# Kernel optimization log

Hardware: AMD Instinct MI355X
Metric: run time of the kernel (lower is better)

The kernel has to match this reference:

```python
import jax, jax.numpy as jnp
import numpy as np

N, E, Z, C, B, G, T = 10000, 160000, 10, 64, 8, 16, 2
R_MAX = 5.0
AVG_NEIGH = 16.0
L_SLICES = ((0, 1), (1, 4), (4, 9))  # l=0,1,2 blocks of the 9 SH components


def sph_harm(u):
    # component-normalized real spherical harmonics up to l=2, u: [E,3] unit vectors
    x, y, z = u[:, 0], u[:, 1], u[:, 2]
    s3, s5, s15 = 3.0 ** 0.5, 5.0 ** 0.5, 15.0 ** 0.5
    return jnp.stack([
        jnp.ones_like(x),
        s3 * x, s3 * y, s3 * z,
        s15 * x * y, s15 * y * z, (s5 / 2) * (3 * z * z - 1), s15 * x * z, (s15 / 2) * (x * x - y * y),
    ], axis=1)  # [E,9]


def radial_embed(r):
    # Bessel basis * polynomial cutoff (p=5), r: [E]
    u = r / R_MAX
    n = jnp.arange(1, B + 1, dtype=jnp.float32)
    bessel = jnp.sqrt(2.0 / R_MAX) * jnp.sin(n[None, :] * jnp.pi * u[:, None]) / (r[:, None] + 1e-9)
    p = 5.0
    fc = 1 - (p + 1) * (p + 2) / 2 * u ** p + p * (p + 2) * u ** (p + 1) - p * (p + 1) / 2 * u ** (p + 2)
    fc = jnp.where(u < 1.0, fc, 0.0)
    return bessel * fc[:, None]  # [E,B]


def per_l_linear(x, W):
    # x: [n,C,9], W: [3,C,C]; independent channel mixing per l-block
    return jnp.concatenate([
        jnp.einsum('ncm,cd->ndm', x[:, :, s:e], W[l]) for l, (s, e) in enumerate(L_SLICES)
    ], axis=2)


def _forward(positions, node_attrs, charges, shifts, W_emb, atomic_energies,
             W_r1, W_r2, W_mix, W_sc, w_poly, W_prod, w_e, w_d,
             edge_index, batch, num_graphs):
    sender, receiver = edge_index[0], edge_index[1]
    # atomic reference energies
    node_e0 = node_attrs @ atomic_energies  # [N]
    e0 = jax.ops.segment_sum(node_e0, batch, num_segments=num_graphs)
    # node embedding: scalars only
    node_feats = jnp.zeros((positions.shape[0], C, 9), positions.dtype)
    node_feats = node_feats.at[:, :, 0].set(node_attrs @ W_emb)
    # edge geometry
    vec = positions[sender] - positions[receiver] + shifts  # [E,3]
    lengths = jnp.sqrt(jnp.sum(vec * vec, axis=1) + 1e-12)
    sh = sph_harm(vec / lengths[:, None])        # [E,9]
    edge_feats = radial_embed(lengths)           # [E,B]
    energies = [e0]
    dipoles = []
    for t in range(T):
        # radial MLP -> per-channel TP weights
        w = jax.nn.silu(edge_feats @ W_r1[t]) @ W_r2[t]      # [E,C]
        h_s = node_feats[sender, :, 0]                       # gather sender scalars [E,C]
        m = (w * h_s)[:, :, None] * sh[:, None, :]           # TP message [E,C,9]
        agg = jax.ops.segment_sum(m, receiver, num_segments=positions.shape[0]) / AVG_NEIGH
        msg = per_l_linear(agg, W_mix[t])
        sc = per_l_linear(node_feats, W_sc[t])               # self-connection
        # product basis (correlation 3): channel-wise scalar polynomial gate
        s0 = msg[:, :, 0]
        poly = w_poly[t, :, 0][None] + w_poly[t, :, 1][None] * s0 + w_poly[t, :, 2][None] * s0 * s0
        node_feats = per_l_linear(msg * poly[:, :, None], W_prod[t]) + sc
        # readout: 1x0e energy + 1x1o dipole
        e_n = node_feats[:, :, 0] @ w_e[t]                   # [N]
        energies.append(jax.ops.segment_sum(e_n, batch, num_segments=num_graphs))
        dipoles.append(jnp.einsum('ncm,c->nm', node_feats[:, :, 1:4], w_d[t]))  # [N,3]
    contributions = jnp.stack(energies, axis=-1)             # [G,T+1]
    total_energy = jnp.sum(contributions, axis=-1)           # [G]
    atomic_dipoles = jnp.sum(jnp.stack(dipoles, axis=-1), axis=-1)  # [N,3]
    total_dipole = jax.ops.segment_sum(atomic_dipoles, batch, num_segments=num_graphs)
    total_dipole = total_dipole + jax.ops.segment_sum(charges[:, None] * positions, batch, num_segments=num_graphs)
    return total_energy, contributions, atomic_dipoles, total_dipole


def setup_inputs():
    key = jax.random.key(0)
    ks = jax.random.split(key, 16)
    s = 0.1
    species = jax.random.randint(ks[1], (N,), 0, Z)
    return {
        'positions': jax.random.normal(ks[0], (N, 3)) * 3.0,
        'node_attrs': jax.nn.one_hot(species, Z, dtype=jnp.float32),
        'charges': jax.random.normal(ks[2], (N,)) * 0.1,
        'shifts': jnp.zeros((E, 3), jnp.float32),
        'W_emb': jax.random.normal(ks[5], (Z, C)) * s,
        'atomic_energies': jax.random.normal(ks[6], (Z,)) * s,
        'W_r1': jax.random.normal(ks[7], (T, B, 64)) * s,
        'W_r2': jax.random.normal(ks[8], (T, 64, C)) * s,
        'W_mix': jax.random.normal(ks[9], (T, 3, C, C)) * s,
        'W_sc': jax.random.normal(ks[10], (T, 3, C, C)) * s,
        'w_poly': jax.random.normal(ks[11], (T, C, 3)) * s,
        'W_prod': jax.random.normal(ks[12], (T, 3, C, C)) * s,
        'w_e': jax.random.normal(ks[13], (T, C)) * s,
        'w_d': jax.random.normal(ks[14], (T, C)) * s,
        'edge_index': jax.random.randint(ks[3], (2, E), 0, N),
        'batch': jnp.sort(jax.random.randint(ks[4], (N,), 0, G)),
        'num_graphs': G,
    }


def reference(positions, node_attrs, charges, shifts, W_emb, atomic_energies,
              W_r1, W_r2, W_mix, W_sc, w_poly, W_prod, w_e, w_d,
              edge_index, batch, num_graphs):
    args = (node_attrs, charges, shifts, W_emb, atomic_energies, W_r1, W_r2,
            W_mix, W_sc, w_poly, W_prod, w_e, w_d, edge_index, batch, num_graphs)
    total_energy, contributions, atomic_dipoles, total_dipole = _forward(positions, *args)
    forces = -jax.grad(lambda p: jnp.sum(_forward(p, *args)[0]))(positions)
    return total_energy, contributions, forces, total_dipole, atomic_dipoles
```

## Files before the change

### kernel.cpp

```cpp
#include <hip/hip_runtime.h>
#include <hip/hip_bf16.h>

#define NN 10000
#define NE 160000
#define NZ 10
#define NBES 8
#define NG 16
#define NT 2
#define NB 2048
#define NB1 2049
#define PL ((size_t)NN*64)

static constexpr float PI_F  = 3.14159265358979323846f;
static constexpr float KBES  = 0.63245553203367587f;
static constexpr float S3    = 1.73205080756887729f;

static constexpr size_t OFF_UVL  = 0;
static constexpr size_t OFF_PIN  = OFF_UVL + (size_t)NE*4;
static constexpr size_t OFF_ATT  = OFF_PIN + (size_t)NN*3;
static constexpr size_t OFF_CHG  = OFF_ATT + (size_t)NN*NZ;
static constexpr size_t OFF_SHF  = OFF_CHG + (size_t)NN;
static constexpr size_t OFF_NF0  = OFF_SHF + (size_t)NE*3;
static constexpr size_t OFF_NF1  = OFF_NF0 + PL;
static constexpr size_t OFF_MSG0 = OFF_NF1 + 4*PL;
static constexpr size_t OFF_MSG1 = OFF_MSG0 + 4*PL;
static constexpr size_t OFF_AGG  = OFF_MSG1 + 4*PL;
static constexpr size_t O_GA1    = OFF_AGG;
static constexpr size_t O_GA0    = OFF_AGG + 2*PL;
static constexpr size_t OFF_W    = OFF_AGG + 4*PL;
static constexpr size_t O_WEMB   = OFF_W;
static constexpr size_t O_AE     = O_WEMB + 640;
static constexpr size_t O_R1     = O_AE   + 16;
static constexpr size_t O_R2     = O_R1   + 1024;
static constexpr size_t O_WMIX   = O_R2   + 8192;
static constexpr size_t O_WMIXT  = O_WMIX + 24576;
static constexpr size_t O_WSC    = O_WMIXT+ 24576;
static constexpr size_t O_WSCT   = O_WSC  + 24576;
static constexpr size_t O_WPROD  = O_WSCT + 24576;
static constexpr size_t O_WPRODT = O_WPROD+ 24576;
static constexpr size_t O_WPOLY  = O_WPRODT+24576;
static constexpr size_t O_WE     = O_WPOLY+ 384;
static constexpr size_t O_WD     = O_WE   + 128;
static constexpr size_t OFF_ACC  = O_WD   + 128;
static constexpr size_t O_E0G    = OFF_ACC;
static constexpr size_t O_ETG    = O_E0G + 16;
static constexpr size_t O_TD     = O_ETG + 32;
static constexpr size_t O_ADP    = O_TD  + 48;
static constexpr size_t O_GPOS   = O_ADP + (size_t)NN*3;
static constexpr size_t ACC_FLOATS = 96 + (size_t)NN*6;
static constexpr size_t O_EN0    = O_GPOS + (size_t)NN*3;
static constexpr size_t O_EN1    = O_EN0 + NN;
static constexpr size_t O_E0N    = O_EN1 + NN;
static constexpr size_t O_FLAG   = O_E0N + NN;
static constexpr size_t O_TW     = O_FLAG + 4;
static constexpr size_t O_TQ     = O_TW + (size_t)2*NB1*64;
static constexpr size_t O_OFFR   = O_TQ + (size_t)2*NB1*64;
static constexpr size_t O_OFFS   = O_OFFR + (NN+1);
static constexpr size_t O_CURR   = O_OFFS + (NN+1);
static constexpr size_t O_CURS   = O_CURR + NN;
static constexpr size_t O_RECRAW = O_CURS + NN;
static constexpr size_t O_RECR   = (O_RECRAW + 7) & ~(size_t)7;
static constexpr size_t O_RECS   = O_RECR + (size_t)NE*8;
static constexpr size_t WS_FLOATS= O_RECS + (size_t)NE*8;

__device__ __forceinline__ float rlane(float v, int l){
  return __int_as_float(__builtin_amdgcn_readlane(__float_as_int(v), l));
}

static constexpr int LD_CNT[14] = {NN*3, NN*NZ, NN, NE*3, NZ*64, NZ, NT*NBES*64, NT*64*64,
                                   NT*3*64*64, NT*3*64*64, NT*64*3, NT*3*64*64, NT*64, NT*64};
static constexpr int LD_TOTAL = NN*3 + NN*NZ + NN + NE*3 + NZ*64 + NZ + NT*NBES*64 + NT*64*64
                              + 3*(NT*3*64*64) + NT*64*3 + 4*(NT*64) - NT*64*2;
__global__ __launch_bounds__(256) void k_load_all(
    const void* s0, const void* s1, const void* s2, const void* s3, const void* s4,
    const void* s5, const void* s6, const void* s7, const void* s8, const void* s9,
    const void* s10, const void* s11, const void* s12, const void* s13,
    float* __restrict__ ws){
  __shared__ int found;
  if (threadIdx.x == 0) found = 0;
  __syncthreads();
  const unsigned* raw = (const unsigned*)s1;
  int f = 0;
  for (int i = threadIdx.x; i < 4096; i += 256){
    unsigned w = raw[i];
    f |= (w == 0x00003F80u || w == 0x3F803F80u) ? 1 : 0;
  }
  if (f) found = 1;
  __syncthreads();
  const int isbf = found;
  if (blockIdx.x == 0 && threadIdx.x == 0) ((int*)(ws + O_FLAG))[0] = isbf;

  const void* srcs[14] = {s0,s1,s2,s3,s4,s5,s6,s7,s8,s9,s10,s11,s12,s13};
  const size_t dsts[14] = {OFF_PIN, OFF_ATT, OFF_CHG, OFF_SHF, O_WEMB, O_AE, O_R1, O_R2,
                           O_WMIX, O_WSC, O_WPOLY, O_WPROD, O_WE, O_WD};
  int i = blockIdx.x*256 + threadIdx.x;
  int seg = -1, off = i;
  #pragma unroll
  for (int j = 0; j < 14; ++j){
    if (seg < 0){
      if (off < LD_CNT[j]) seg = j;
      else off -= LD_CNT[j];
    }
  }
  if (seg < 0) return;
  float v = isbf ? __bfloat162float(((const __hip_bfloat16*)srcs[seg])[off])
                 : ((const float*)srcs[seg])[off];
  ws[dsts[seg] + off] = v;
}

__global__ void k_transpose_all(float* __restrict__ ws){
  const size_t srcs[3] = {O_WMIX, O_WSC, O_WPROD};
  const size_t dsts[3] = {O_WMIXT, O_WSCT, O_WPRODT};
  int i = blockIdx.x*256 + threadIdx.x;
  if (i >= 18*4096) return;
  int mm = i >> 12, r = (i >> 6) & 63, c = i & 63;
  int grp = mm / 6, m = mm % 6;
  ws[dsts[grp] + (size_t)m*4096 + (size_t)c*64 + r] =
      ws[srcs[grp] + (size_t)m*4096 + (size_t)r*64 + c];
}

static constexpr int GEOM_B = (NE+255)/256;
static constexpr int TAB_B  = (2*NB1+3)/4;
static constexpr int INIT_B = (NN+3)/4;
__global__ __launch_bounds__(256, 3) void k_prep(float* __restrict__ ws, const int* __restrict__ ei){
  int b = blockIdx.x;
  if (b < GEOM_B){
    int e = b*256 + threadIdx.x;
    if (e >= NE) return;
    const float* pos = ws + OFF_PIN;
    const float* shifts = ws + OFF_SHF;
    int s = ei[e], r = ei[NE + e];
    float vx = pos[s*3+0] - pos[r*3+0] + shifts[(size_t)e*3+0];
    float vy = pos[s*3+1] - pos[r*3+1] + shifts[(size_t)e*3+1];
    float vz = pos[s*3+2] - pos[r*3+2] + shifts[(size_t)e*3+2];
    float L = sqrtf(vx*vx + vy*vy + vz*vz + 1e-12f);
    float inv = 1.f / L;
    float4 uq; uq.x = vx*inv; uq.y = vy*inv; uq.z = vz*inv; uq.w = L;
    *(float4*)(ws + OFF_UVL + (size_t)e*4) = uq;
    if (L < 5.f){
      atomicAdd((int*)(ws + O_CURR) + r, 1);
      atomicAdd((int*)(ws + O_CURS) + s, 1);
    }
  } else if (b < GEOM_B + TAB_B){
    int lane = threadIdx.x & 63;
    int task = (b - GEOM_B)*4 + (threadIdx.x >> 6);
    if (task >= 2*NB1) return;
    int t = task / NB1, node = task % NB1;
    const float* R1 = ws + O_R1 + (size_t)t*512;
    const float* R2 = ws + O_R2 + (size_t)t*4096;
    float r1c[8];
    #pragma unroll
    for (int j = 0; j < 8; ++j) r1c[j] = R1[j*64 + lane];
    float L = fmaxf((float)node * (5.f/NB), 1e-6f);
    float ur = L*0.2f;
    float ef[8], dd[8];
    if (ur < 1.f){
      float u2=ur*ur, u4=u2*u2, u5=u4*ur;
      float fc = 1.f - 21.f*u5 + 35.f*u5*ur - 15.f*u5*u2;
      float omu = 1.f - ur;
      float dfc = -105.f*u4*omu*omu;
      float invr = 1.f/(L + 1e-9f);
      #pragma unroll
      for (int bb = 0; bb < 8; ++bb){
        float nb = (float)(bb+1);
        float arg = nb*PI_F*ur;
        float sn = __sinf(arg), cs = __cosf(arg);
        float bes = KBES*sn*invr;
        float dbes = KBES*(nb*PI_F*0.2f)*cs*invr - bes*invr;
        ef[bb] = bes*fc;
        dd[bb] = dbes*fc + bes*dfc*0.2f;
      }
    } else {
      #pragma unroll
      for (int bb = 0; bb < 8; ++bb){ ef[bb] = 0.f; dd[bb] = 0.f; }
    }
    float a = 0.f, tt = 0.f;
    #pragma unroll
    for (int bb = 0; bb < 8; ++bb){ a = fmaf(ef[bb], r1c[bb], a); tt = fmaf(r1c[bb], dd[bb], tt); }
    float sg = 1.f/(1.f + __expf(-a));
    float sl = a*sg;
    float q  = sg*fmaf(a, 1.f - sg, 1.f)*tt;
    float r2c[64];
    #pragma unroll
    for (int j = 0; j < 64; ++j) r2c[j] = R2[j*64 + lane];
    float W0=0.f, W1=0.f, Q0=0.f, Q1=0.f;
    #pragma unroll
    for (int j = 0; j < 64; j += 2){
      W0 = fmaf(rlane(sl, j  ), r2c[j  ], W0);
      W1 = fmaf(rlane(sl, j+1), r2c[j+1], W1);
      Q0 = fmaf(rlane(q,  j  ), r2c[j  ], Q0);
      Q1 = fmaf(rlane(q,  j+1), r2c[j+1], Q1);
    }
    size_t idx = ((size_t)t*NB1 + node)*64 + lane;
    ws[O_TW + idx] = (W0+W1)*(1.f/16.f);
    ws[O_TQ + idx] = (Q0+Q1)*(1.f/16.f);
  } else {
    int lane = threadIdx.x & 63;
    int n = (b - GEOM_B - TAB_B)*4 + (threadIdx.x >> 6);
    if (n >= NN) return;
    const float* attrs = ws + OFF_ATT;
    float acc = 0.f;
    #pragma unroll
    for (int z = 0; z < NZ; ++z) acc = fmaf(attrs[(size_t)n*NZ+z], ws[O_WEMB + z*64 + lane], acc);
    ws[OFF_NF0 + (size_t)n*64 + lane] = acc;
    if (lane == 0){
      float e = 0.f;
      #pragma unroll
      for (int z = 0; z < NZ; ++z) e = fmaf(attrs[(size_t)n*NZ+z], ws[O_AE + z], e);
      ws[O_E0N + n] = e;
    }
  }
}

__global__ __launch_bounds__(1024) void k_csr_scan(
    int* __restrict__ curr, int* __restrict__ curs,
    int* __restrict__ offr, int* __restrict__ offs_){
  __shared__ unsigned short cr[NN], cs[NN];
  __shared__ int pr[1024], ps[1024];
  int tid = threadIdx.x;
  for (int i = tid; i < NN; i += 1024){
    cr[i] = (unsigned short)curr[i];
    cs[i] = (unsigned short)curs[i];
  }
  __syncthreads();
  const int chunk = (NN + 1023)/1024;
  int lo = tid*chunk, hi = lo + chunk;
  if (hi > NN) hi = NN;
  if (lo > NN) lo = NN;
  int sr = 0, ss = 0;
  for (int i = lo; i < hi; ++i){ sr += cr[i]; ss += cs[i]; }
  pr[tid] = sr; ps[tid] = ss;
  __syncthreads();
  for (int o = 1; o < 1024; o <<= 1){
    int vr = (tid >= o) ? pr[tid-o] : 0;
    int vs = (tid >= o) ? ps[tid-o] : 0;
    __syncthreads();
    pr[tid] += vr; ps[tid] += vs;
    __syncthreads();
  }
  int runr = tid ? pr[tid-1] : 0;
  int runs = tid ? ps[tid-1] : 0;
  for (int i = lo; i < hi; ++i){
    int a = cr[i], c = cs[i];
    offr[i] = runr; curr[i] = runr; runr += a;
    offs_[i] = runs; curs[i] = runs; runs += c;
  }
  if (tid == 1023){ offr[NN] = runr; offs_[NN] = runs; }
}

__global__ void k_csr_fill(const int* __restrict__ ei, const float* __restrict__ uvl,
                           int* __restrict__ curr, int* __restrict__ curs,
                           float* __restrict__ recr, float* __restrict__ recs){
  int e = blockIdx.x*256 + threadIdx.x;
  if (e >= NE) return;
  float4 q = *(const float4*)(uvl + (size_t)e*4);
  if (q.w >= 5.f) return;
  int s = ei[e], r = ei[NE + e];
  int4 meta; meta.x = s; meta.y = r; meta.z = e; meta.w = 0;
  int pr = atomicAdd(&curr[r], 1);
  *(float4*)(recr + (size_t)pr*8) = q;
  *(int4*)(recr + (size_t)pr*8 + 4) = meta;
  int ps = atomicAdd(&curs[s], 1);
  *(float4*)(recs + (size_t)ps*8) = q;
  *(int4*)(recs + (size_t)ps*8 + 4) = meta;
}

__global__ __launch_bounds__(256) void k_agg(
    const float* __restrict__ TWt, const float* __restrict__ recr,
    const float* __restrict__ h, const int* __restrict__ offr,
    float* __restrict__ agg){
  int lane = threadIdx.x & 63;
  int wid = blockIdx.x*4 + (threadIdx.x >> 6);
  int nw  = gridDim.x*4;
  for (int n = wid; n < NN; n += nw){
    int lo = offr[n], hi = offr[n+1];
    float c0=0.f, x1=0.f, y1=0.f, z1=0.f;
    float d0=0.f, x2=0.f, y2=0.f, z2=0.f;
    int i = lo;
    for (; i+1 < hi; i += 2){
      const float4 qa = *(const float4*)(recr + (size_t)i*8);
      const int sa = __builtin_amdgcn_readfirstlane(((const int*)(recr + (size_t)i*8 + 4))[0]);
      const float4 qb = *(const float4*)(recr + (size_t)(i+1)*8);
      const int sb = __builtin_amdgcn_readfirstlane(((const int*)(recr + (size_t)(i+1)*8 + 4))[0]);
      float pa = qa.w*(NB/5.f); int ba = (int)pa; float fa = pa - (float)ba;
      float pb = qb.w*(NB/5.f); int bbq = (int)pb; float fb = pb - (float)bbq;
      const float* Ta = TWt + (size_t)ba*64 + lane;
      const float* Tb = TWt + (size_t)bbq*64 + lane;
      float ta0 = Ta[0], tb0 = Tb[0];
      float wa = fmaf(Ta[64]-ta0, fa, ta0);
      float wb = fmaf(Tb[64]-tb0, fb, tb0);
      float wha = wa * h[(size_t)sa*64 + lane];
      float whb = wb * h[(size_t)sb*64 + lane];
      c0 += wha; d0 += whb;
      x1 = fmaf(wha, qa.x, x1); x2 = fmaf(whb, qb.x, x2);
      y1 = fmaf(wha, qa.y, y1); y2 = fmaf(whb, qb.y, y2);
      z1 = fmaf(wha, qa.z, z1); z2 = fmaf(whb, qb.z, z2);
    }
    if (i < hi){
      const float4 q = *(const float4*)(recr + (size_t)i*8);
      const int sU = __builtin_amdgcn_readfirstlane(((const int*)(recr + (size_t)i*8 + 4))[0]);
      float pa = q.w*(NB/5.f); int ba = (int)pa; float fa = pa - (float)ba;
      const float* Ta = TWt + (size_t)ba*64 + lane;
      float ta0 = Ta[0];
      float wa = fmaf(Ta[64]-ta0, fa, ta0);
      float wha = wa * h[(size_t)sU*64 + lane];
      c0 += wha;
      x1 = fmaf(wha, q.x, x1);
      y1 = fmaf(wha, q.y, y1);
      z1 = fmaf(wha, q.z, z1);
    }
    size_t ob = (size_t)n*64 + lane;
    agg[ob]        = c0 + d0;
    agg[ob+PL]     = S3*(x1 + x2);
    agg[ob+2*PL]   = S3*(y1 + y2);
    agg[ob+3*PL]   = S3*(z1 + z2);
  }
}

__global__ __launch_bounds__(256, 3) void k_lin2(
    const float* __restrict__ in, const float* __restrict__ W3, float* __restrict__ out){
  int k = blockIdx.y;
  int l = (k==0) ? 0 : 1;
  const float* W = W3 + (size_t)l*4096;
  int lane = threadIdx.x & 63;
  float wcol[64];
  #pragma unroll
  for (int j = 0; j < 64; ++j) wcol[j] = W[j*64 + lane];
  int wid = blockIdx.x*4 + (threadIdx.x >> 6);
  int nw  = gridDim.x*4;
  const float* inp = in + (size_t)k*PL;
  float* outp = out + (size_t)k*PL;
  for (int n = wid; n < NN; n += nw){
    float x = inp[(size_t)n*64 + lane];
    float a0 = 0.f, a1 = 0.f, a2 = 0.f, a3 = 0.f;
    #pragma unroll
    for (int j = 0; j < 64; j += 4){
      a0 = fmaf(rlane(x, j  ), wcol[j  ], a0);
      a1 = fmaf(rlane(x, j+1), wcol[j+1], a1);
      a2 = fmaf(rlane(x, j+2), wcol[j+2], a2);
      a3 = fmaf(rlane(x, j+3), wcol[j+3], a3);
    }
    outp[(size_t)n*64 + lane] = (a0+a1) + (a2+a3);
  }
}

template<int WRITE_NF, int NF_SINGLE>
__global__ __launch_bounds__(256, 3) void k_tail(
    const float* __restrict__ nf_in, const float* __restrict__ msg,
    const float* __restrict__ Wsc, const float* __restrict__ Wprod, const float* __restrict__ wp,
    const float* __restrict__ we, const float* __restrict__ wd,
    float* __restrict__ nf_out, float* __restrict__ en, float* __restrict__ adp){
  int lane = threadIdx.x & 63;
  int k = threadIdx.x >> 6;
  int l = (k==0) ? 0 : 1;
  const bool use_sc = !(NF_SINGLE && k > 0);
  float wcs[64], wcp[64];
  #pragma unroll
  for (int j = 0; j < 64; ++j)
    wcp[j] = Wprod[(size_t)l*4096 + j*64 + lane];
  if (use_sc){
    #pragma unroll
    for (int j = 0; j < 64; ++j)
      wcs[j] = Wsc[(size_t)l*4096 + j*64 + lane];
  }
  float p0 = wp[lane*3], p1 = wp[lane*3+1], p2 = wp[lane*3+2];
  float rw = (k==0) ? we[lane] : wd[lane];
  const float* msgk = msg + (size_t)k*PL;
  const float* nfk  = nf_in + (size_t)k*PL;
  float* outk = nf_out + (size_t)k*PL;
  for (int n = blockIdx.x; n < NN; n += gridDim.x){
    size_t base = (size_t)n*64 + lane;
    float s0 = msg[base];
    float xm = (k==0) ? s0 : msgk[base];
    float xg = xm * fmaf(fmaf(p2, s0, p1), s0, p0);
    float b0=0.f, b1=0.f;
    #pragma unroll
    for (int j = 0; j < 64; j += 2){
      b0 = fmaf(rlane(xg, j  ), wcp[j  ], b0);
      b1 = fmaf(rlane(xg, j+1), wcp[j+1], b1);
    }
    float out = b0 + b1;
    if (use_sc){
      float xs = nfk[base];
      float a0=0.f, a1=0.f;
      #pragma unroll
      for (int j = 0; j < 64; j += 2){
        a0 = fmaf(rlane(xs, j  ), wcs[j  ], a0);
        a1 = fmaf(rlane(xs, j+1), wcs[j+1], a1);
      }
      out += a0 + a1;
    }
    if (WRITE_NF) outk[base] = out;
    float red = out * rw;
    #pragma unroll
    for (int o = 32; o; o >>= 1) red += __shfl_xor(red, o, 64);
    if (lane == 0){
      if (k == 0) en[n] = red;
      else        adp[n*3 + (k-1)] += red;
    }
  }
}

__global__ __launch_bounds__(256, 3) void k_gback1(
    const float* __restrict__ WPRODT1, const float* __restrict__ we1,
    const float* __restrict__ msg1, const float* __restrict__ wp,
    const float* __restrict__ WMIXT1, float* __restrict__ out){
  int lane = threadIdx.x & 63;
  float wcol[64];
  #pragma unroll
  for (int j = 0; j < 64; ++j) wcol[j] = WMIXT1[j*64 + lane];
  float g = 0.f;
  #pragma unroll
  for (int c = 0; c < 64; ++c) g = fmaf(we1[c], WPRODT1[c*64 + lane], g);
  float p0 = wp[lane*3], p1 = wp[lane*3+1], p2 = wp[lane*3+2];
  int wid = blockIdx.x*4 + (threadIdx.x >> 6);
  int nw  = gridDim.x*4;
  for (int n = wid; n < NN; n += nw){
    float s0 = msg1[(size_t)n*64 + lane];
    float poly = fmaf(fmaf(p2, s0, p1), s0, p0);
    float dp   = fmaf(2.f*p2, s0, p1);
    float gb = g*fmaf(s0, dp, poly);
    float a0=0.f, a1=0.f, a2=0.f, a3=0.f;
    #pragma unroll
    for (int j = 0; j < 64; j += 4){
      a0 = fmaf(rlane(gb, j  ), wcol[j  ], a0);
      a1 = fmaf(rlane(gb, j+1), wcol[j+1], a1);
      a2 = fmaf(rlane(gb, j+2), wcol[j+2], a2);
      a3 = fmaf(rlane(gb, j+3), wcol[j+3], a3);
    }
    out[(size_t)n*64 + lane] = (a0+a1) + (a2+a3);
  }
}

__global__ __launch_bounds__(256) void k_ghg0(float* __restrict__ ws, const int* __restrict__ offs_){
  __shared__ float wl[2*4096];
  for (int i = threadIdx.x; i < 4096; i += 256){
    wl[i]        = ws[O_WPRODT + i];
    wl[4096 + i] = ws[O_WMIXT + i];
  }
  __syncthreads();
  const int lane = threadIdx.x & 63;
  int wid = blockIdx.x*4 + (threadIdx.x >> 6);
  const int nw = gridDim.x*4;
  float gnfc = ws[O_WE + lane];
  {
    const float* WS1 = ws + O_WSCT + 12288;
    const float* we1 = ws + O_WE + 64;
    #pragma unroll
    for (int c = 0; c < 64; ++c) gnfc = fmaf(we1[c], WS1[c*64 + lane], gnfc);
  }
  const float p0 = ws[O_WPOLY + lane*3];
  const float p1 = ws[O_WPOLY + lane*3 + 1];
  const float p2 = ws[O_WPOLY + lane*3 + 2];
  const float* TW1 = ws + O_TW + (size_t)NB1*64;
  const float* recs = ws + O_RECS;
  const float* GA1 = ws + O_GA1;
  for (int n = wid; n < NN; n += nw){
    int lo = offs_[n], hi = offs_[n+1];
    float acc = 0.f, acc2 = 0.f;
    int i = lo;
    for (; i+1 < hi; i += 2){
      const float4 qa = *(const float4*)(recs + (size_t)i*8);
      const int ra = __builtin_amdgcn_readfirstlane(((const int*)(recs + (size_t)i*8 + 4))[1]);
      const float4 qb = *(const float4*)(recs + (size_t)(i+1)*8);
      const int rb = __builtin_amdgcn_readfirstlane(((const int*)(recs + (size_t)(i+1)*8 + 4))[1]);
      float pa = qa.w*(NB/5.f); int ba = (int)pa; float fa = pa - (float)ba;
      float pb = qb.w*(NB/5.f); int bbq = (int)pb; float fb = pb - (float)bbq;
      const float* Ta = TW1 + (size_t)ba*64 + lane;
      const float* Tb = TW1 + (size_t)bbq*64 + lane;
      float ta0 = Ta[0], tb0 = Tb[0];
      float wa = fmaf(Ta[64]-ta0, fa, ta0);
      float wb = fmaf(Tb[64]-tb0, fb, tb0);
      acc  = fmaf(wa, GA1[(size_t)ra*64 + lane], acc);
      acc2 = fmaf(wb, GA1[(size_t)rb*64 + lane], acc2);
    }
    if (i < hi){
      const float4 q = *(const float4*)(recs + (size_t)i*8);
      const int rU = __builtin_amdgcn_readfirstlane(((const int*)(recs + (size_t)i*8 + 4))[1]);
      float pa = q.w*(NB/5.f); int ba = (int)pa; float fa = pa - (float)ba;
      const float* Ta = TW1 + (size_t)ba*64 + lane;
      float ta0 = Ta[0];
      float wa = fmaf(Ta[64]-ta0, fa, ta0);
      acc = fmaf(wa, GA1[(size_t)rU*64 + lane], acc);
    }
    float gB = gnfc + (acc + acc2);
    float q0=0.f, q1=0.f;
    #pragma unroll
    for (int j = 0; j < 64; j += 2){
      q0 = fmaf(rlane(gB,j),   wl[j*64 + lane],     q0);
      q1 = fmaf(rlane(gB,j+1), wl[(j+1)*64 + lane], q1);
    }
    float gmp = q0 + q1;
    float s0v = ws[OFF_MSG0 + (size_t)n*64 + lane];
    float poly = fmaf(fmaf(p2, s0v, p1), s0v, p0);
    float dp   = fmaf(2.f*p2, s0v, p1);
    float gb = gmp * fmaf(s0v, dp, poly);
    float u0=0.f, u1=0.f;
    #pragma unroll
    for (int j = 0; j < 64; j += 2){
      u0 = fmaf(rlane(gb,j),   wl[4096 + j*64 + lane],     u0);
      u1 = fmaf(rlane(gb,j+1), wl[4096 + (j+1)*64 + lane], u1);
    }
    ws[O_GA0 + (size_t)n*64 + lane] = u0 + u1;
  }
}

__global__ __launch_bounds__(256) void k_bwdE2(float* __restrict__ ws, const int* __restrict__ nlive_ptr){
  const int lane = threadIdx.x & 63;
  int wid = blockIdx.x*4 + (threadIdx.x >> 6);
  const int nw = gridDim.x*4;
  const int nlive = nlive_ptr[0];
  const float* recs = ws + O_RECS;
  const float* TQ  = ws + O_TQ;
  const float* h0  = ws + OFF_NF0;
  const float* h1  = ws + OFF_NF1;
  const float* ga0 = ws + O_GA0;
  const float* ga1 = ws + O_GA1;
  float* gpos = ws + O_GPOS;
  for (int i = wid; i < nlive; i += nw){
    const float4 q = *(const float4*)(recs + (size_t)i*8);
    const int* meta = (const int*)(recs + (size_t)i*8 + 4);
    const int s = __builtin_amdgcn_readfirstlane(meta[0]);
    const int r = __builtin_amdgcn_readfirstlane(meta[1]);
    float posb = q.w*(NB/5.f);
    int bi = (int)posb;
    float fr = posb - (float)bi;
    const float* T0 = TQ + (size_t)bi*64 + lane;
    const float* T1 = T0 + (size_t)NB1*64;
    float Q0 = fmaf(T0[64]-T0[0], fr, T0[0]);
    float Q1 = fmaf(T1[64]-T1[0], fr, T1[0]);
    float rr = Q0*h0[(size_t)s*64 + lane]*ga0[(size_t)r*64 + lane]
             + Q1*h1[(size_t)s*64 + lane]*ga1[(size_t)r*64 + lane];
    #pragma unroll
    for (int o = 32; o; o >>= 1) rr += __shfl_xor(rr, o, 64);
    if (lane < 3){
      float u = (lane==0) ? q.x : ((lane==1) ? q.y : q.z);
      float v = rr*u;
      atomicAdd(&gpos[(size_t)s*3 + lane],  v);
      atomicAdd(&gpos[(size_t)r*3 + lane], -v);
    }
  }
}

__global__ void k_reduce(const float* __restrict__ e0n, const float* __restrict__ en0,
                         const float* __restrict__ en1, const float* __restrict__ adp,
                         const float* __restrict__ q, const float* __restrict__ pos,
                         const int* __restrict__ batch, float* __restrict__ e0g,
                         float* __restrict__ Etg, float* __restrict__ td){
  int n = blockIdx.x*256 + threadIdx.x;
  int lane = threadIdx.x & 63;
  bool valid = (n < NN);
  int g = valid ? batch[n] : -1;
  float v0=0.f, v1=0.f, v2=0.f, tx=0.f, ty=0.f, tz=0.f;
  if (valid){
    v0 = e0n[n]; v1 = en0[n]; v2 = en1[n];
    float qq = q[n];
    tx = adp[n*3+0] + qq*pos[n*3+0];
    ty = adp[n*3+1] + qq*pos[n*3+1];
    tz = adp[n*3+2] + qq*pos[n*3+2];
  }
  int g0 = __shfl(g, 0, 64), g63 = __shfl(g, 63, 64);
  if (g0 == g63 && g0 >= 0){
    #pragma unroll
    for (int o = 32; o; o >>= 1){
      v0 += __shfl_xor(v0, o, 64); v1 += __shfl_xor(v1, o, 64); v2 += __shfl_xor(v2, o, 64);
      tx += __shfl_xor(tx, o, 64); ty += __shfl_xor(ty, o, 64); tz += __shfl_xor(tz, o, 64);
    }
    if (lane == 0){
      atomicAdd(&e0g[g0], v0); atomicAdd(&Etg[g0], v1); atomicAdd(&Etg[16+g0], v2);
      atomicAdd(&td[g0*3+0], tx); atomicAdd(&td[g0*3+1], ty); atomicAdd(&td[g0*3+2], tz);
    }
  } else if (valid){
    atomicAdd(&e0g[g], v0); atomicAdd(&Etg[g], v1); atomicAdd(&Etg[16+g], v2);
    atomicAdd(&td[g*3+0], tx); atomicAdd(&td[g*3+1], ty); atomicAdd(&td[g*3+2], tz);
  }
}

__global__ void k_writeout(const float* __restrict__ e0g, const float* __restrict__ Etg,
                           const float* __restrict__ td, const float* __restrict__ adp,
                           const float* __restrict__ gpos, void* __restrict__ outv,
                           const int* __restrict__ flag){
  int i = blockIdx.x*256 + threadIdx.x;
  const int total = NG + NG*3 + NN*3 + NG*3 + NN*3;
  if (i >= total) return;
  float v;
  if (i < 16){
    v = e0g[i] + Etg[i] + Etg[16+i];
  } else if (i < 64){
    int j = i - 16; int g = j/3, t = j - g*3;
    v = (t == 0) ? e0g[g] : Etg[(t-1)*16 + g];
  } else if (i < 64 + NN*3){
    v = -gpos[i-64];
  } else if (i < 64 + NN*3 + 48){
    v = td[i - (64 + NN*3)];
  } else {
    v = adp[i - (64 + NN*3 + 48)];
  }
  if (flag[0]) ((__hip_bfloat16*)outv)[i] = __float2bfloat16(v);
  else         ((float*)outv)[i] = v;
}

extern "C" void kernel_launch(void* const* d_in, const int* in_sizes, int n_in,
                              void* d_out, int out_size, void* d_ws, size_t ws_size,
                              hipStream_t stream) {
  if (ws_size < WS_FLOATS*sizeof(float)) return;
  const int* ei    = (const int*)d_in[14];
  const int* batch = (const int*)d_in[15];
  float* ws = (float*)d_ws;

  int* offr  = (int*)(ws + O_OFFR);
  int* offs_ = (int*)(ws + O_OFFS);
  int* curr  = (int*)(ws + O_CURR);
  int* curs  = (int*)(ws + O_CURS);

  hipMemsetAsync(ws + OFF_ACC, 0, ACC_FLOATS*sizeof(float), stream);
  hipMemsetAsync(curr, 0, 2*NN*sizeof(int), stream);

  k_load_all<<<(LD_TOTAL+255)/256, 256, 0, stream>>>(
      d_in[0], d_in[1], d_in[2], d_in[3], d_in[4], d_in[5], d_in[6], d_in[7],
      d_in[8], d_in[9], d_in[10], d_in[11], d_in[12], d_in[13], ws);
  k_transpose_all<<<288, 256, 0, stream>>>(ws);
  k_prep<<<GEOM_B + TAB_B + INIT_B, 256, 0, stream>>>(ws, ei);
  k_csr_scan<<<1, 1024, 0, stream>>>(curr, curs, offr, offs_);
  k_csr_fill<<<(NE+255)/256, 256, 0, stream>>>(ei, ws+OFF_UVL, curr, curs,
                                               ws+O_RECR, ws+O_RECS);

  const size_t NF[2]  = {OFF_NF0, OFF_NF1};
  const size_t MSG[2] = {OFF_MSG0, OFF_MSG1};
  dim3 ling(256, 4);

  for (int t = 0; t < NT; ++t){
    k_agg<<<1024, 256, 0, stream>>>(ws+O_TW + (size_t)t*NB1*64, ws+O_RECR,
                                    ws+NF[t], offr, ws+OFF_AGG);
    k_lin2<<<ling, 256, 0, stream>>>(ws+OFF_AGG, ws+O_WMIX + (size_t)t*12288, ws+MSG[t]);
    if (t == 0){
      k_tail<1,1><<<1024, 256, 0, stream>>>(ws+NF[0], ws+MSG[0],
                                            ws+O_WSC, ws+O_WPROD,
                                            ws+O_WPOLY, ws+O_WE, ws+O_WD,
                                            ws+OFF_NF1, ws+O_EN0, ws+O_ADP);
    } else {
      k_tail<0,0><<<1024, 256, 0, stream>>>(ws+NF[1], ws+MSG[1],
                                            ws+O_WSC + 12288, ws+O_WPROD + 12288,
                                            ws+O_WPOLY + 192, ws+O_WE + 64, ws+O_WD + 64,
                                            ws+OFF_NF1, ws+O_EN1, ws+O_ADP);
    }
  }

  k_gback1<<<1024, 256, 0, stream>>>(ws+O_WPRODT+12288, ws+O_WE+64,
                                     ws+OFF_MSG1, ws+O_WPOLY+192,
                                     ws+O_WMIXT+12288, ws+O_GA1);
  k_ghg0<<<1024, 256, 0, stream>>>(ws, offs_);
  k_bwdE2<<<2048, 256, 0, stream>>>(ws, offs_ + NN);

  k_reduce<<<(NN+255)/256, 256, 0, stream>>>(ws+O_E0N, ws+O_EN0, ws+O_EN1, ws+O_ADP,
                                             ws+OFF_CHG, ws+OFF_PIN, batch,
                                             ws+O_E0G, ws+O_ETG, ws+O_TD);
  k_writeout<<<(60112+255)/256, 256, 0, stream>>>(ws+O_E0G, ws+O_ETG, ws+O_TD, ws+O_ADP,
                                                  ws+O_GPOS, d_out, (const int*)(ws+O_FLAG));
}
```

Before: 335.9 us.

## Fuse transpose, gback1 and reduce kernels into neighbors; pair edges in bwdE2

The weight transpose moves into k_prep as extra blocks, and it now transposes only the five matrices actually used. The layer-1 gradient backprop (k_gback1) is fused into the layer-1 k_lin2 for the scalar block, so msg1 is consumed while it is still in registers. The per-graph reduction (k_reduce) becomes extra blocks of k_ghg0, and the workspace layout is remapped so ga1 no longer collides with agg. k_bwdE2 processes two edges per wave iteration to expose more memory-level parallelism. Together these remove three launches and one global read pass, at the cost of higher register pressure in k_lin2.

```diff
diff --git a/kernel.cpp b/kernel.cpp
--- a/kernel.cpp
+++ b/kernel.cpp
@@ -25,8 +25,8 @@
 static constexpr size_t OFF_MSG0 = OFF_NF1 + 4*PL;
 static constexpr size_t OFF_MSG1 = OFF_MSG0 + 4*PL;
 static constexpr size_t OFF_AGG  = OFF_MSG1 + 4*PL;
-static constexpr size_t O_GA1    = OFF_AGG;
-static constexpr size_t O_GA0    = OFF_AGG + 2*PL;
+static constexpr size_t O_GA1    = OFF_MSG0 + PL;
+static constexpr size_t O_GA0    = OFF_AGG;
 static constexpr size_t OFF_W    = OFF_AGG + 4*PL;
 static constexpr size_t O_WEMB   = OFF_W;
 static constexpr size_t O_AE     = O_WEMB + 640;
@@ -108,20 +108,10 @@
   ws[dsts[seg] + off] = v;
 }
 
-__global__ void k_transpose_all(float* __restrict__ ws){
-  const size_t srcs[3] = {O_WMIX, O_WSC, O_WPROD};
-  const size_t dsts[3] = {O_WMIXT, O_WSCT, O_WPRODT};
-  int i = blockIdx.x*256 + threadIdx.x;
-  if (i >= 18*4096) return;
-  int mm = i >> 12, r = (i >> 6) & 63, c = i & 63;
-  int grp = mm / 6, m = mm % 6;
-  ws[dsts[grp] + (size_t)m*4096 + (size_t)c*64 + r] =
-      ws[srcs[grp] + (size_t)m*4096 + (size_t)r*64 + c];
-}
-
 static constexpr int GEOM_B = (NE+255)/256;
 static constexpr int TAB_B  = (2*NB1+3)/4;
 static constexpr int INIT_B = (NN+3)/4;
+static constexpr int TRAN_B = 5*4096/256;
 __global__ __launch_bounds__(256, 3) void k_prep(float* __restrict__ ws, const int* __restrict__ ei){
   int b = blockIdx.x;
   if (b < GEOM_B){
@@ -194,7 +184,7 @@
     size_t idx = ((size_t)t*NB1 + node)*64 + lane;
     ws[O_TW + idx] = (W0+W1)*(1.f/16.f);
     ws[O_TQ + idx] = (Q0+Q1)*(1.f/16.f);
-  } else {
+  } else if (b < GEOM_B + TAB_B + INIT_B){
     int lane = threadIdx.x & 63;
     int n = (b - GEOM_B - TAB_B)*4 + (threadIdx.x >> 6);
     if (n >= NN) return;
@@ -209,6 +199,12 @@
       for (int z = 0; z < NZ; ++z) e = fmaf(attrs[(size_t)n*NZ+z], ws[O_AE + z], e);
       ws[O_E0N + n] = e;
     }
+  } else {
+    int i = (b - GEOM_B - TAB_B - INIT_B)*256 + threadIdx.x;
+    int mat = i >> 12, r = (i >> 6) & 63, c = i & 63;
+    const size_t src[5] = {O_WMIX, O_WMIX+12288, O_WPROD, O_WPROD+12288, O_WSC+12288};
+    const size_t dst[5] = {O_WMIXT, O_WMIXT+12288, O_WPRODT, O_WPRODT+12288, O_WSCT+12288};
+    ws[dst[mat] + (size_t)c*64 + r] = ws[src[mat] + (size_t)r*64 + c];
   }
 }
 
@@ -317,8 +313,12 @@
   }
 }
 
+template<int GB1>
 __global__ __launch_bounds__(256, 3) void k_lin2(
-    const float* __restrict__ in, const float* __restrict__ W3, float* __restrict__ out){
+    const float* __restrict__ in, const float* __restrict__ W3, float* __restrict__ out,
+    const float* __restrict__ WMIXT1, const float* __restrict__ WPRODT1,
+    const float* __restrict__ we1, const float* __restrict__ wp1,
+    float* __restrict__ ga1){
   int k = blockIdx.y;
   int l = (k==0) ? 0 : 1;
   const float* W = W3 + (size_t)l*4096;
@@ -326,6 +326,16 @@
   float wcol[64];
   #pragma unroll
   for (int j = 0; j < 64; ++j) wcol[j] = W[j*64 + lane];
+  float wcol2[64];
+  float g = 0.f, p0 = 0.f, p1 = 0.f, p2 = 0.f;
+  const bool gb1 = GB1 && (k == 0);
+  if (gb1){
+    #pragma unroll
+    for (int j = 0; j < 64; ++j) wcol2[j] = WMIXT1[j*64 + lane];
+    #pragma unroll
+    for (int c = 0; c < 64; ++c) g = fmaf(we1[c], WPRODT1[c*64 + lane], g);
+    p0 = wp1[lane*3]; p1 = wp1[lane*3+1]; p2 = wp1[lane*3+2];
+  }
   int wid = blockIdx.x*4 + (threadIdx.x >> 6);
   int nw  = gridDim.x*4;
   const float* inp = in + (size_t)k*PL;
@@ -340,7 +350,22 @@
       a2 = fmaf(rlane(x, j+2), wcol[j+2], a2);
       a3 = fmaf(rlane(x, j+3), wcol[j+3], a3);
     }
-    outp[(size_t)n*64 + lane] = (a0+a1) + (a2+a3);
+    float m = (a0+a1) + (a2+a3);
+    outp[(size_t)n*64 + lane] = m;
+    if (gb1){
+      float poly = fmaf(fmaf(p2, m, p1), m, p0);
+      float dp   = fmaf(2.f*p2, m, p1);
+      float gb = g*fmaf(m, dp, poly);
+      float b0=0.f, b1=0.f, b2=0.f, b3=0.f;
+      #pragma unroll
+      for (int j = 0; j < 64; j += 4){
+        b0 = fmaf(rlane(gb, j  ), wcol2[j  ], b0);
+        b1 = fmaf(rlane(gb, j+1), wcol2[j+1], b1);
+        b2 = fmaf(rlane(gb, j+2), wcol2[j+2], b2);
+        b3 = fmaf(rlane(gb, j+3), wcol2[j+3], b3);
+      }
+      ga1[(size_t)n*64 + lane] = (b0+b1) + (b2+b3);
+    }
   }
 }
 
@@ -401,39 +426,42 @@
   }
 }
 
-__global__ __launch_bounds__(256, 3) void k_gback1(
-    const float* __restrict__ WPRODT1, const float* __restrict__ we1,
-    const float* __restrict__ msg1, const float* __restrict__ wp,
-    const float* __restrict__ WMIXT1, float* __restrict__ out){
-  int lane = threadIdx.x & 63;
-  float wcol[64];
-  #pragma unroll
-  for (int j = 0; j < 64; ++j) wcol[j] = WMIXT1[j*64 + lane];
-  float g = 0.f;
-  #pragma unroll
-  for (int c = 0; c < 64; ++c) g = fmaf(we1[c], WPRODT1[c*64 + lane], g);
-  float p0 = wp[lane*3], p1 = wp[lane*3+1], p2 = wp[lane*3+2];
-  int wid = blockIdx.x*4 + (threadIdx.x >> 6);
-  int nw  = gridDim.x*4;
-  for (int n = wid; n < NN; n += nw){
-    float s0 = msg1[(size_t)n*64 + lane];
-    float poly = fmaf(fmaf(p2, s0, p1), s0, p0);
-    float dp   = fmaf(2.f*p2, s0, p1);
-    float gb = g*fmaf(s0, dp, poly);
-    float a0=0.f, a1=0.f, a2=0.f, a3=0.f;
-    #pragma unroll
-    for (int j = 0; j < 64; j += 4){
-      a0 = fmaf(rlane(gb, j  ), wcol[j  ], a0);
-      a1 = fmaf(rlane(gb, j+1), wcol[j+1], a1);
-      a2 = fmaf(rlane(gb, j+2), wcol[j+2], a2);
-      a3 = fmaf(rlane(gb, j+3), wcol[j+3], a3);
-    }
-    out[(size_t)n*64 + lane] = (a0+a1) + (a2+a3);
-  }
-}
-
-__global__ __launch_bounds__(256) void k_ghg0(float* __restrict__ ws, const int* __restrict__ offs_){
+static constexpr int GHG_GRID = 1024;
+static constexpr int RED_B = (NN+255)/256;
+__global__ __launch_bounds__(256) void k_ghg0(float* __restrict__ ws, const int* __restrict__ offs_,
+                                              const int* __restrict__ batch){
   __shared__ float wl[2*4096];
+  if (blockIdx.x >= GHG_GRID){
+    int n = (blockIdx.x - GHG_GRID)*256 + threadIdx.x;
+    int lane = threadIdx.x & 63;
+    bool valid = (n < NN);
+    int g = valid ? batch[n] : -1;
+    float v0=0.f, v1=0.f, v2=0.f, tx=0.f, ty=0.f, tz=0.f;
+    if (valid){
+      v0 = ws[O_E0N + n]; v1 = ws[O_EN0 + n]; v2 = ws[O_EN1 + n];
+      float qq = ws[OFF_CHG + n];
+      tx = ws[O_ADP + n*3+0] + qq*ws[OFF_PIN + n*3+0];
+      ty = ws[O_ADP + n*3+1] + qq*ws[OFF_PIN + n*3+1];
+      tz = ws[O_ADP + n*3+2] + qq*ws[OFF_PIN + n*3+2];
+    }
+    float* e0g = ws + O_E0G; float* Etg = ws + O_ETG; float* td = ws + O_TD;
+    int g0 = __shfl(g, 0, 64), g63 = __shfl(g, 63, 64);
+    if (g0 == g63 && g0 >= 0){
+      #pragma unroll
+      for (int o = 32; o; o >>= 1){
+        v0 += __shfl_xor(v0, o, 64); v1 += __shfl_xor(v1, o, 64); v2 += __shfl_xor(v2, o, 64);
+        tx += __shfl_xor(tx, o, 64); ty += __shfl_xor(ty, o, 64); tz += __shfl_xor(tz, o, 64);
+      }
+      if (lane == 0){
+        atomicAdd(&e0g[g0], v0); atomicAdd(&Etg[g0], v1); atomicAdd(&Etg[16+g0], v2);
+        atomicAdd(&td[g0*3+0], tx); atomicAdd(&td[g0*3+1], ty); atomicAdd(&td[g0*3+2], tz);
+      }
+    } else if (valid){
+      atomicAdd(&e0g[g], v0); atomicAdd(&Etg[g], v1); atomicAdd(&Etg[16+g], v2);
+      atomicAdd(&td[g*3+0], tx); atomicAdd(&td[g*3+1], ty); atomicAdd(&td[g*3+2], tz);
+    }
+    return;
+  }
   for (int i = threadIdx.x; i < 4096; i += 256){
     wl[i]        = ws[O_WPRODT + i];
     wl[4096 + i] = ws[O_WMIXT + i];
@@ -441,7 +469,7 @@
   __syncthreads();
   const int lane = threadIdx.x & 63;
   int wid = blockIdx.x*4 + (threadIdx.x >> 6);
-  const int nw = gridDim.x*4;
+  const int nw = GHG_GRID*4;
   float gnfc = ws[O_WE + lane];
   {
     const float* WS1 = ws + O_WSCT + 12288;
@@ -517,62 +545,53 @@
   const float* ga0 = ws + O_GA0;
   const float* ga1 = ws + O_GA1;
   float* gpos = ws + O_GPOS;
-  for (int i = wid; i < nlive; i += nw){
-    const float4 q = *(const float4*)(recs + (size_t)i*8);
-    const int* meta = (const int*)(recs + (size_t)i*8 + 4);
-    const int s = __builtin_amdgcn_readfirstlane(meta[0]);
-    const int r = __builtin_amdgcn_readfirstlane(meta[1]);
-    float posb = q.w*(NB/5.f);
-    int bi = (int)posb;
-    float fr = posb - (float)bi;
-    const float* T0 = TQ + (size_t)bi*64 + lane;
-    const float* T1 = T0 + (size_t)NB1*64;
-    float Q0 = fmaf(T0[64]-T0[0], fr, T0[0]);
-    float Q1 = fmaf(T1[64]-T1[0], fr, T1[0]);
-    float rr = Q0*h0[(size_t)s*64 + lane]*ga0[(size_t)r*64 + lane]
-             + Q1*h1[(size_t)s*64 + lane]*ga1[(size_t)r*64 + lane];
-    #pragma unroll
-    for (int o = 32; o; o >>= 1) rr += __shfl_xor(rr, o, 64);
+  for (int i = wid; i < nlive; i += 2*nw){
+    const int i2 = i + nw;
+    const bool hasB = (i2 < nlive);
+    const float4 qA = *(const float4*)(recs + (size_t)i*8);
+    const int* mA = (const int*)(recs + (size_t)i*8 + 4);
+    const int sA = __builtin_amdgcn_readfirstlane(mA[0]);
+    const int rA = __builtin_amdgcn_readfirstlane(mA[1]);
+    float pA = qA.w*(NB/5.f); int bA = (int)pA; float fA = pA - (float)bA;
+    const float* T0A = TQ + (size_t)bA*64 + lane;
+    const float* T1A = T0A + (size_t)NB1*64;
+    float Q0A = fmaf(T0A[64]-T0A[0], fA, T0A[0]);
+    float Q1A = fmaf(T1A[64]-T1A[0], fA, T1A[0]);
+    float rrA = Q0A*h0[(size_t)sA*64 + lane]*ga0[(size_t)rA*64 + lane]
+              + Q1A*h1[(size_t)sA*64 + lane]*ga1[(size_t)rA*64 + lane];
+    float rrB = 0.f;
+    float4 qB; qB.x = 0.f; qB.y = 0.f; qB.z = 0.f; qB.w = 0.f;
+    int sB = 0, rB = 0;
+    if (hasB){
+      qB = *(const float4*)(recs + (size_t)i2*8);
+      const int* mB = (const int*)(recs + (size_t)i2*8 + 4);
+      sB = __builtin_amdgcn_readfirstlane(mB[0]);
+      rB = __builtin_amdgcn_readfirstlane(mB[1]);
+      float pB = qB.w*(NB/5.f); int bB = (int)pB; float fB = pB - (float)bB;
+      const float* T0B = TQ + (size_t)bB*64 + lane;
+      const float* T1B = T0B + (size_t)NB1*64;
+      float Q0B = fmaf(T0B[64]-T0B[0], fB, T0B[0]);
+      float Q1B = fmaf(T1B[64]-T1B[0], fB, T1B[0]);
+      rrB = Q0B*h0[(size_t)sB*64 + lane]*ga0[(size_t)rB*64 + lane]
+          + Q1B*h1[(size_t)sB*64 + lane]*ga1[(size_t)rB*64 + lane];
+    }
+    #pragma unroll
+    for (int o = 32; o; o >>= 1){
+      rrA += __shfl_xor(rrA, o, 64);
+      rrB += __shfl_xor(rrB, o, 64);
+    }
     if (lane < 3){
-      float u = (lane==0) ? q.x : ((lane==1) ? q.y : q.z);
-      float v = rr*u;
-      atomicAdd(&gpos[(size_t)s*3 + lane],  v);
-      atomicAdd(&gpos[(size_t)r*3 + lane], -v);
-    }
-  }
-}
-
-__global__ void k_reduce(const float* __restrict__ e0n, const float* __restrict__ en0,
-                         const float* __restrict__ en1, const float* __restrict__ adp,
-                         const float* __restrict__ q, const float* __restrict__ pos,
-                         const int* __restrict__ batch, float* __restrict__ e0g,
-                         float* __restrict__ Etg, float* __restrict__ td){
-  int n = blockIdx.x*256 + threadIdx.x;
-  int lane = threadIdx.x & 63;
-  bool valid = (n < NN);
-  int g = valid ? batch[n] : -1;
-  float v0=0.f, v1=0.f, v2=0.f, tx=0.f, ty=0.f, tz=0.f;
-  if (valid){
-    v0 = e0n[n]; v1 = en0[n]; v2 = en1[n];
-    float qq = q[n];
-    tx = adp[n*3+0] + qq*pos[n*3+0];
-    ty = adp[n*3+1] + qq*pos[n*3+1];
-    tz = adp[n*3+2] + qq*pos[n*3+2];
-  }
-  int g0 = __shfl(g, 0, 64), g63 = __shfl(g, 63, 64);
-  if (g0 == g63 && g0 >= 0){
-    #pragma unroll
-    for (int o = 32; o; o >>= 1){
-      v0 += __shfl_xor(v0, o, 64); v1 += __shfl_xor(v1, o, 64); v2 += __shfl_xor(v2, o, 64);
-      tx += __shfl_xor(tx, o, 64); ty += __shfl_xor(ty, o, 64); tz += __shfl_xor(tz, o, 64);
-    }
-    if (lane == 0){
-      atomicAdd(&e0g[g0], v0); atomicAdd(&Etg[g0], v1); atomicAdd(&Etg[16+g0], v2);
-      atomicAdd(&td[g0*3+0], tx); atomicAdd(&td[g0*3+1], ty); atomicAdd(&td[g0*3+2], tz);
-    }
-  } else if (valid){
-    atomicAdd(&e0g[g], v0); atomicAdd(&Etg[g], v1); atomicAdd(&Etg[16+g], v2);
-    atomicAdd(&td[g*3+0], tx); atomicAdd(&td[g*3+1], ty); atomicAdd(&td[g*3+2], tz);
+      float uA = (lane==0) ? qA.x : ((lane==1) ? qA.y : qA.z);
+      float vA = rrA*uA;
+      atomicAdd(&gpos[(size_t)sA*3 + lane],  vA);
+      atomicAdd(&gpos[(size_t)rA*3 + lane], -vA);
+      if (hasB){
+        float uB = (lane==0) ? qB.x : ((lane==1) ? qB.y : qB.z);
+        float vB = rrB*uB;
+        atomicAdd(&gpos[(size_t)sB*3 + lane],  vB);
+        atomicAdd(&gpos[(size_t)rB*3 + lane], -vB);
+      }
+    }
   }
 }
 
@@ -619,42 +638,32 @@
   k_load_all<<<(LD_TOTAL+255)/256, 256, 0, stream>>>(
       d_in[0], d_in[1], d_in[2], d_in[3], d_in[4], d_in[5], d_in[6], d_in[7],
       d_in[8], d_in[9], d_in[10], d_in[11], d_in[12], d_in[13], ws);
-  k_transpose_all<<<288, 256, 0, stream>>>(ws);
-  k_prep<<<GEOM_B + TAB_B + INIT_B, 256, 0, stream>>>(ws, ei);
+  k_prep<<<GEOM_B + TAB_B + INIT_B + TRAN_B, 256, 0, stream>>>(ws, ei);
   k_csr_scan<<<1, 1024, 0, stream>>>(curr, curs, offr, offs_);
   k_csr_fill<<<(NE+255)/256, 256, 0, stream>>>(ei, ws+OFF_UVL, curr, curs,
                                                ws+O_RECR, ws+O_RECS);
 
-  const size_t NF[2]  = {OFF_NF0, OFF_NF1};
-  const size_t MSG[2] = {OFF_MSG0, OFF_MSG1};
   dim3 ling(256, 4);
 
-  for (int t = 0; t < NT; ++t){
-    k_agg<<<1024, 256, 0, stream>>>(ws+O_TW + (size_t)t*NB1*64, ws+O_RECR,
-                                    ws+NF[t], offr, ws+OFF_AGG);
-    k_lin2<<<ling, 256, 0, stream>>>(ws+OFF_AGG, ws+O_WMIX + (size_t)t*12288, ws+MSG[t]);
-    if (t == 0){
-      k_tail<1,1><<<1024, 256, 0, stream>>>(ws+NF[0], ws+MSG[0],
-                                            ws+O_WSC, ws+O_WPROD,
-                                            ws+O_WPOLY, ws+O_WE, ws+O_WD,
-                                            ws+OFF_NF1, ws+O_EN0, ws+O_ADP);
-    } else {
-      k_tail<0,0><<<1024, 256, 0, stream>>>(ws+NF[1], ws+MSG[1],
-                                            ws+O_WSC + 12288, ws+O_WPROD + 12288,
-                                            ws+O_WPOLY + 192, ws+O_WE + 64, ws+O_WD + 64,
-                                            ws+OFF_NF1, ws+O_EN1, ws+O_ADP);
-    }
-  }
-
-  k_gback1<<<1024, 256, 0, stream>>>(ws+O_WPRODT+12288, ws+O_WE+64,
-                                     ws+OFF_MSG1, ws+O_WPOLY+192,
-                                     ws+O_WMIXT+12288, ws+O_GA1);
-  k_ghg0<<<1024, 256, 0, stream>>>(ws, offs_);
+  k_agg<<<1024, 256, 0, stream>>>(ws+O_TW, ws+O_RECR, ws+OFF_NF0, offr, ws+OFF_AGG);
+  k_lin2<0><<<ling, 256, 0, stream>>>(ws+OFF_AGG, ws+O_WMIX, ws+OFF_MSG0,
+                                      ws, ws, ws, ws, ws);
+  k_tail<1,1><<<1024, 256, 0, stream>>>(ws+OFF_NF0, ws+OFF_MSG0,
+                                        ws+O_WSC, ws+O_WPROD,
+                                        ws+O_WPOLY, ws+O_WE, ws+O_WD,
+                                        ws+OFF_NF1, ws+O_EN0, ws+O_ADP);
+  k_agg<<<1024, 256, 0, stream>>>(ws+O_TW + (size_t)NB1*64, ws+O_RECR, ws+OFF_NF1, offr, ws+OFF_AGG);
+  k_lin2<1><<<ling, 256, 0, stream>>>(ws+OFF_AGG, ws+O_WMIX + 12288, ws+OFF_MSG1,
+                                      ws+O_WMIXT + 12288, ws+O_WPRODT + 12288,
+                                      ws+O_WE + 64, ws+O_WPOLY + 192, ws+O_GA1);
+  k_tail<0,0><<<1024, 256, 0, stream>>>(ws+OFF_NF1, ws+OFF_MSG1,
+                                        ws+O_WSC + 12288, ws+O_WPROD + 12288,
+                                        ws+O_WPOLY + 192, ws+O_WE + 64, ws+O_WD + 64,
+                                        ws+OFF_NF1, ws+O_EN1, ws+O_ADP);
+
+  k_ghg0<<<GHG_GRID + RED_B, 256, 0, stream>>>(ws, offs_, batch);
   k_bwdE2<<<2048, 256, 0, stream>>>(ws, offs_ + NN);
 
-  k_reduce<<<(NN+255)/256, 256, 0, stream>>>(ws+O_E0N, ws+O_EN0, ws+O_EN1, ws+O_ADP,
-                                             ws+OFF_CHG, ws+OFF_PIN, batch,
-                                             ws+O_E0G, ws+O_ETG, ws+O_TD);
   k_writeout<<<(60112+255)/256, 256, 0, stream>>>(ws+O_E0G, ws+O_ETG, ws+O_TD, ws+O_ADP,
                                                   ws+O_GPOS, d_out, (const int*)(ws+O_FLAG));
 }
```

After: 338.5 us. Within noise of the previous version (+0.8%).
